# Kernel tuning notes

Measured on AMD Instinct MI355X. Metric: run time of the kernel, lower is better.

Reference implementation:

```python
import jax, jax.numpy as jnp
import numpy as np

D = 768
H = 8
DH = D // H
SCALE = DH ** -0.5


def layer_norm(x, g, b, eps=1e-5):
    mu = jnp.mean(x, axis=-1, keepdims=True)
    var = jnp.var(x, axis=-1, keepdims=True)
    return (x - mu) * jax.lax.rsqrt(var + eps) * g + b


def setup_inputs() -> dict:
    key = jax.random.key(0)
    ks = jax.random.split(key, 8)
    B, N = 8, 1024
    s = lambda fan_in: 1.0 / np.sqrt(fan_in)
    return {
        "x": jax.random.normal(ks[0], (B, N, D), jnp.float32),
        "w_qkv": jax.random.normal(ks[1], (D, 3 * D), jnp.float32) * s(D),
        "w_o": jax.random.normal(ks[2], (D, D), jnp.float32) * s(D),
        "b_o": jnp.zeros((D,), jnp.float32),
        "w1": jax.random.normal(ks[3], (D, 4 * D), jnp.float32) * s(D),
        "b1": jnp.zeros((4 * D,), jnp.float32),
        "w2": jax.random.normal(ks[4], (4 * D, D), jnp.float32) * s(4 * D),
        "b2": jnp.zeros((D,), jnp.float32),
        "g1": jnp.ones((D,), jnp.float32), "be1": jnp.zeros((D,), jnp.float32),
        "gm": jnp.ones((D,), jnp.float32), "bm": jnp.zeros((D,), jnp.float32),
        "g3": jnp.ones((D,), jnp.float32), "be3": jnp.zeros((D,), jnp.float32),
    }


def reference(x, w_qkv, w_o, b_o, w1, b1, w2, b2, g1, be1, gm, bm, g3, be3):
    B, N, _ = x.shape
    # --- attention branch (pre-norm) ---
    h = layer_norm(x, g1, be1)
    qkv = h @ w_qkv                                   # (B,N,3D)
    qkv = qkv.reshape(B, N, 3, H, DH).transpose(2, 0, 3, 1, 4)  # (3,B,H,N,Dh)
    q, k, v = qkv[0], qkv[1], qkv[2]
    att = jax.nn.softmax(jnp.einsum('bhnd,bhmd->bhnm', q, k) * SCALE, axis=-1)
    o = jnp.einsum('bhnm,bhmd->bhnd', att, v)         # (B,H,N,Dh)
    # faithful to original: reshape WITHOUT transposing heads back
    o = o.reshape(B, N, D)
    o = o @ w_o + b_o
    x = o + x
    # --- MLP branch (has its own pre-norm; GELU after BOTH linears; dropout off) ---
    h = layer_norm(x, gm, bm)
    h = jax.nn.gelu(h @ w1 + b1, approximate=False)
    h = jax.nn.gelu(h @ w2 + b2, approximate=False)
    x = h + x
    return layer_norm(x, g3, be3)
```

## Files before the change

kernel.cpp:

```cpp
#include <hip/hip_runtime.h>
#include <cmath>
#include <cstdint>

typedef __bf16 bf16;
typedef __bf16 bf16x8 __attribute__((ext_vector_type(8)));
typedef __bf16 bf16x4 __attribute__((ext_vector_type(4)));
typedef float  f32x4  __attribute__((ext_vector_type(4)));

#define M_TOK 8192
#define SCALE_ 0.10206207261596575f

__device__ __forceinline__ void gld_lds16(const void* g, void* l) {
  __builtin_amdgcn_global_load_lds(
      (__attribute__((address_space(1))) void*)(uintptr_t)g,
      (__attribute__((address_space(3))) void*)(uintptr_t)l,
      16, 0, 0);
}

__device__ __forceinline__ float gelu_f(float x) {
  float u = x * (0.7978845608f + 0.0356774081f * x * x);
  float t = 1.0f - 2.0f / (__expf(2.0f * u) + 1.0f);
  return 0.5f * x * (1.0f + t);
}

__global__ __launch_bounds__(256) void make_frags_kernel(
    const float* __restrict__ w_qkv, const float* __restrict__ w_o,
    const float* __restrict__ w1, const float* __restrict__ w2,
    bf16* __restrict__ fqkv, bf16* __restrict__ fwo, bf16* __restrict__ fw1,
    bf16* __restrict__ fw2) {
  int chunk = blockIdx.x * 4 + (threadIdx.x >> 6);
  int lane = threadIdx.x & 63;
  const float* src;
  bf16* dst;
  int K, N, base;
  if (chunk < 3456) {
    src = w_qkv; dst = fqkv; K = 768; N = 2304; base = 0;
  } else if (chunk < 4608) {
    src = w_o; dst = fwo; K = 768; N = 768; base = 3456;
  } else if (chunk < 9216) {
    src = w1; dst = fw1; K = 768; N = 3072; base = 4608;
  } else {
    src = w2; dst = fw2; K = 3072; N = 768; base = 9216;
  }
  int lid = chunk - base;
  int kc = K / 32;
  int n16 = lid / kc, c = lid - n16 * kc;
  int lr = lane & 15, qd = lane >> 4;
  int n = n16 * 16 + lr;
  int k0 = c * 32 + qd * 8;
  bf16x8 v;
#pragma unroll
  for (int e = 0; e < 8; e++) v[e] = (bf16)src[(size_t)(k0 + e) * N + n];
  *(bf16x8*)&dst[(size_t)lid * 512 + lane * 8] = v;
}

__global__ __launch_bounds__(256) void ln_kernel(
    const float* __restrict__ x, const float* __restrict__ g,
    const float* __restrict__ b, bf16* __restrict__ ob) {
  int w = threadIdx.x >> 6, lane = threadIdx.x & 63;
  size_t row = (size_t)blockIdx.x * 4 + w;
  const float* xr = x + row * 768;
  float4 v[3];
  float s = 0.f, sq = 0.f;
#pragma unroll
  for (int k = 0; k < 3; k++) {
    v[k] = *(const float4*)(xr + (k * 64 + lane) * 4);
    s += v[k].x + v[k].y + v[k].z + v[k].w;
    sq += v[k].x * v[k].x + v[k].y * v[k].y + v[k].z * v[k].z + v[k].w * v[k].w;
  }
#pragma unroll
  for (int off = 32; off >= 1; off >>= 1) {
    s += __shfl_xor(s, off);
    sq += __shfl_xor(sq, off);
  }
  float mean = s * (1.f / 768.f);
  float rstd = rsqrtf(sq * (1.f / 768.f) - mean * mean + 1e-5f);
#pragma unroll
  for (int k = 0; k < 3; k++) {
    int c = (k * 64 + lane) * 4;
    float4 gg = *(const float4*)(g + c);
    float4 bb = *(const float4*)(b + c);
    bf16x4 pk = {(bf16)((v[k].x - mean) * rstd * gg.x + bb.x),
                 (bf16)((v[k].y - mean) * rstd * gg.y + bb.y),
                 (bf16)((v[k].z - mean) * rstd * gg.z + bb.z),
                 (bf16)((v[k].w - mean) * rstd * gg.w + bb.w)};
    *(bf16x4*)(ob + row * 768 + c) = pk;
  }
}

__global__ __launch_bounds__(256) void ln2_reduce_kernel(
    const bf16* __restrict__ p, const float* __restrict__ bo,
    const float* __restrict__ xres, const float* __restrict__ g,
    const float* __restrict__ b, bf16* __restrict__ x2,
    bf16* __restrict__ h2) {
  int w = threadIdx.x >> 6, lane = threadIdx.x & 63;
  size_t row = (size_t)blockIdx.x * 4 + w;
  const bf16* p0 = p + row * 768;
  const bf16* p1 = p0 + (size_t)M_TOK * 768;
  const float* xr = xres + row * 768;
  float4 v[3];
  float s = 0.f, sq = 0.f;
#pragma unroll
  for (int k = 0; k < 3; k++) {
    int c = (k * 64 + lane) * 4;
    bf16x4 a0 = *(const bf16x4*)(p0 + c);
    bf16x4 a1 = *(const bf16x4*)(p1 + c);
    float4 bb = *(const float4*)(bo + c);
    float4 rr = *(const float4*)(xr + c);
    v[k].x = (float)a0[0] + (float)a1[0] + bb.x + rr.x;
    v[k].y = (float)a0[1] + (float)a1[1] + bb.y + rr.y;
    v[k].z = (float)a0[2] + (float)a1[2] + bb.z + rr.z;
    v[k].w = (float)a0[3] + (float)a1[3] + bb.w + rr.w;
    bf16x4 xo = {(bf16)v[k].x, (bf16)v[k].y, (bf16)v[k].z, (bf16)v[k].w};
    *(bf16x4*)(x2 + row * 768 + c) = xo;
    s += v[k].x + v[k].y + v[k].z + v[k].w;
    sq += v[k].x * v[k].x + v[k].y * v[k].y + v[k].z * v[k].z + v[k].w * v[k].w;
  }
#pragma unroll
  for (int off = 32; off >= 1; off >>= 1) {
    s += __shfl_xor(s, off);
    sq += __shfl_xor(sq, off);
  }
  float mean = s * (1.f / 768.f);
  float rstd = rsqrtf(sq * (1.f / 768.f) - mean * mean + 1e-5f);
#pragma unroll
  for (int k = 0; k < 3; k++) {
    int c = (k * 64 + lane) * 4;
    float4 gg = *(const float4*)(g + c);
    float4 bb = *(const float4*)(b + c);
    bf16x4 pk = {(bf16)((v[k].x - mean) * rstd * gg.x + bb.x),
                 (bf16)((v[k].y - mean) * rstd * gg.y + bb.y),
                 (bf16)((v[k].z - mean) * rstd * gg.z + bb.z),
                 (bf16)((v[k].w - mean) * rstd * gg.w + bb.w)};
    *(bf16x4*)(h2 + row * 768 + c) = pk;
  }
}

__global__ __launch_bounds__(256) void ln3_reduce_kernel(
    const bf16* __restrict__ p, const float* __restrict__ b2,
    const bf16* __restrict__ x2, const float* __restrict__ g,
    const float* __restrict__ b, float* __restrict__ out) {
  int w = threadIdx.x >> 6, lane = threadIdx.x & 63;
  size_t row = (size_t)blockIdx.x * 4 + w;
  const bf16* p0 = p + row * 768;
  const bf16* p1 = p0 + (size_t)M_TOK * 768;
  const bf16* xr = x2 + row * 768;
  float4 v[3];
  float s = 0.f, sq = 0.f;
#pragma unroll
  for (int k = 0; k < 3; k++) {
    int c = (k * 64 + lane) * 4;
    bf16x4 a0 = *(const bf16x4*)(p0 + c);
    bf16x4 a1 = *(const bf16x4*)(p1 + c);
    float4 bb = *(const float4*)(b2 + c);
    bf16x4 rr = *(const bf16x4*)(xr + c);
    v[k].x = gelu_f((float)a0[0] + (float)a1[0] + bb.x) + (float)rr[0];
    v[k].y = gelu_f((float)a0[1] + (float)a1[1] + bb.y) + (float)rr[1];
    v[k].z = gelu_f((float)a0[2] + (float)a1[2] + bb.z) + (float)rr[2];
    v[k].w = gelu_f((float)a0[3] + (float)a1[3] + bb.w) + (float)rr[3];
    s += v[k].x + v[k].y + v[k].z + v[k].w;
    sq += v[k].x * v[k].x + v[k].y * v[k].y + v[k].z * v[k].z + v[k].w * v[k].w;
  }
#pragma unroll
  for (int off = 32; off >= 1; off >>= 1) {
    s += __shfl_xor(s, off);
    sq += __shfl_xor(sq, off);
  }
  float mean = s * (1.f / 768.f);
  float rstd = rsqrtf(sq * (1.f / 768.f) - mean * mean + 1e-5f);
#pragma unroll
  for (int k = 0; k < 3; k++) {
    int c = (k * 64 + lane) * 4;
    float4 gg = *(const float4*)(g + c);
    float4 bb = *(const float4*)(b + c);
    float4 ov = {(v[k].x - mean) * rstd * gg.x + bb.x,
                 (v[k].y - mean) * rstd * gg.y + bb.y,
                 (v[k].z - mean) * rstd * gg.z + bb.z,
                 (v[k].w - mean) * rstd * gg.w + bb.w};
    *(float4*)(out + row * 768 + c) = ov;
  }
}

template <int EPI, int LDA, int KT, int KSL, int NN>
__global__ __launch_bounds__(256) void gemm_bt_kernel(
    const bf16* __restrict__ A, const bf16* __restrict__ Bf,
    const float* __restrict__ bias, bf16* __restrict__ outb,
    bf16* __restrict__ qo, bf16* __restrict__ ko, bf16* __restrict__ vto) {
  __shared__ __align__(16) bf16 As[2][128 * 32];
  int tid = threadIdx.x;
  int wave = tid >> 6, lane = tid & 63;
  int qd = lane >> 4, lr = lane & 15;
  int bm0 = blockIdx.x * 128, bn0 = blockIdx.y * 128;
  int wm = (wave >> 1) * 64, wn = (wave & 1) * 64;
  int kbase = blockIdx.z * KSL;
  const int STEPS = KSL / 32;
  const int KC = KT / 32;

  f32x4 acc[4][4] = {};

  int srow = lane >> 2;
  int scol = ((lane & 3) ^ ((lane >> 3) & 3)) * 8;
  const bf16* Ag = A + (size_t)(bm0 + wave * 32 + srow) * LDA + kbase + scol;
  const bf16* Ag2 = Ag + (size_t)16 * LDA;
  int rk = (lr >> 1) & 3;

  const bf16* Bfb =
      Bf + ((size_t)((bn0 + wn) >> 4) * KC + (kbase >> 5)) * 512 + lane * 8;

  auto stage = [&](int c, int buf) {
    char* Al = (char*)As[buf] + wave * 2048;
    gld_lds16(Ag + c * 32, Al);
    gld_lds16(Ag2 + c * 32, Al + 1024);
  };

  stage(0, 0);
  int cur = 0;
#pragma unroll 4
  for (int c = 0; c < STEPS; c++) {
    __syncthreads();
    if (c + 1 < STEPS) stage(c + 1, cur ^ 1);
    bf16x8 breg[4];
#pragma unroll
    for (int jn = 0; jn < 4; jn++)
      breg[jn] = *(const bf16x8*)(Bfb + ((size_t)jn * KC + c) * 512);
    const bf16* Asr = As[cur];
    bf16x8 af[4];
#pragma unroll
    for (int i = 0; i < 4; i++)
      af[i] = *(const bf16x8*)&Asr[(wm + i * 16 + lr) * 32 + ((qd ^ rk) * 8)];
#pragma unroll
    for (int i = 0; i < 4; i++)
#pragma unroll
      for (int j = 0; j < 4; j++)
        acc[i][j] = __builtin_amdgcn_mfma_f32_16x16x32_bf16(af[i], breg[j],
                                                            acc[i][j], 0, 0, 0);
    cur ^= 1;
  }

  bf16* outbs = (EPI == 5) ? outb + (size_t)blockIdx.z * M_TOK * NN : outb;

#pragma unroll
  for (int i = 0; i < 4; i++) {
#pragma unroll
    for (int j = 0; j < 4; j++) {
      if (EPI == 4) {
        int colt = bn0 + wn + j * 16;
        int which = colt / 768;
        int rem = colt - which * 768;
        int h = rem / 96;
        int dhb = rem - h * 96;
        int row0 = bm0 + wm + i * 16 + qd * 4;
        int b = row0 >> 10, n0 = row0 & 1023;
        int bh = b * 8 + h;
        if (which == 2) {
          bf16x4 pk = {(bf16)acc[i][j][0], (bf16)acc[i][j][1],
                       (bf16)acc[i][j][2], (bf16)acc[i][j][3]};
          *(bf16x4*)(vto + ((size_t)(bh * 96 + dhb + lr)) * 1024 + n0) = pk;
        } else if (which == 0) {
#pragma unroll
          for (int r = 0; r < 4; r++)
            qo[((size_t)bh * 1024 + n0 + r) * 96 + dhb + lr] =
                (bf16)(acc[i][j][r] * SCALE_);
        } else {
#pragma unroll
          for (int r = 0; r < 4; r++)
            ko[((size_t)bh * 1024 + n0 + r) * 96 + dhb + lr] =
                (bf16)acc[i][j][r];
        }
      } else {
#pragma unroll
        for (int r = 0; r < 4; r++) {
          int row = bm0 + wm + i * 16 + qd * 4 + r;
          int col = bn0 + wn + j * 16 + lr;
          size_t o = (size_t)row * NN + col;
          float v = acc[i][j][r];
          if (EPI == 2) {
            outbs[o] = (bf16)gelu_f(v + bias[col]);
          } else {
            outbs[o] = (bf16)v;
          }
        }
      }
    }
  }
}

__global__ __launch_bounds__(256) void attn_kernel(
    const bf16* __restrict__ qb, const bf16* __restrict__ kb,
    const bf16* __restrict__ vtb, bf16* __restrict__ operm) {
  __shared__ __align__(16) bf16 Ks[2][64 * 104];
  __shared__ __align__(16) bf16 Vs[2][96 * 72];
  __shared__ __align__(16) bf16 Ps[128 * 72];
  int t = threadIdx.x;
  int w = t >> 6, lane = t & 63;
  int qd = lane >> 4, lr = lane & 15;
  int bh = blockIdx.x, nt0 = blockIdx.y * 128;
  int bq = bh >> 3, hh = bh & 7;

  const bf16* kgb = kb + (size_t)bh * 1024 * 96;
  const bf16* vgb = vtb + (size_t)bh * 96 * 1024;

  bf16x8 kreg[3], vreg[3];
#pragma unroll
  for (int it = 0; it < 3; it++) {
    int idx = it * 256 + t;
    kreg[it] = *(const bf16x8*)(kgb + (idx / 12) * 96 + (idx % 12) * 8);
    vreg[it] = *(const bf16x8*)(vgb + (size_t)(idx >> 3) * 1024 + (idx & 7) * 8);
  }

  const bf16* qg = qb + ((size_t)bh * 1024 + nt0 + w * 32) * 96;
  bf16x8 afq[2][3];
#pragma unroll
  for (int i = 0; i < 2; i++)
#pragma unroll
    for (int ks = 0; ks < 3; ks++)
      afq[i][ks] = *(const bf16x8*)(qg + (i * 16 + lr) * 96 + ks * 32 + qd * 8);

  f32x4 oacc[2][6] = {};
  float lst[2][4] = {};

  int cur = 0;
  for (int kt = 0; kt < 16; kt++) {
#pragma unroll
    for (int it = 0; it < 3; it++) {
      int idx = it * 256 + t;
      *(bf16x8*)&Ks[cur][(idx / 12) * 104 + (idx % 12) * 8] = kreg[it];
      *(bf16x8*)&Vs[cur][(idx >> 3) * 72 + (idx & 7) * 8] = vreg[it];
    }
    if (kt < 15) {
      const bf16* kg = kgb + (size_t)(kt + 1) * 64 * 96;
      const bf16* vg = vgb + (kt + 1) * 64;
#pragma unroll
      for (int it = 0; it < 3; it++) {
        int idx = it * 256 + t;
        kreg[it] = *(const bf16x8*)(kg + (idx / 12) * 96 + (idx % 12) * 8);
        vreg[it] =
            *(const bf16x8*)(vg + (size_t)(idx >> 3) * 1024 + (idx & 7) * 8);
      }
    }
    __syncthreads();

    f32x4 sacc[2][4] = {};
#pragma unroll
    for (int ks = 0; ks < 3; ks++) {
      bf16x8 bk[4];
#pragma unroll
      for (int jn = 0; jn < 4; jn++)
        bk[jn] =
            *(const bf16x8*)&Ks[cur][(jn * 16 + lr) * 104 + ks * 32 + qd * 8];
#pragma unroll
      for (int i = 0; i < 2; i++)
#pragma unroll
        for (int jn = 0; jn < 4; jn++)
          sacc[i][jn] = __builtin_amdgcn_mfma_f32_16x16x32_bf16(
              afq[i][ks], bk[jn], sacc[i][jn], 0, 0, 0);
    }

#pragma unroll
    for (int i = 0; i < 2; i++)
#pragma unroll
      for (int jn = 0; jn < 4; jn++)
#pragma unroll
        for (int r = 0; r < 4; r++) {
          float p = __expf(sacc[i][jn][r]);
          lst[i][r] += p;
          Ps[(w * 32 + i * 16 + qd * 4 + r) * 72 + jn * 16 + lr] = (bf16)p;
        }

#pragma unroll
    for (int ks = 0; ks < 2; ks++) {
      bf16x8 ap[2];
#pragma unroll
      for (int i = 0; i < 2; i++)
        ap[i] =
            *(const bf16x8*)&Ps[(w * 32 + i * 16 + lr) * 72 + ks * 32 + qd * 8];
#pragma unroll
      for (int jn = 0; jn < 6; jn++) {
        bf16x8 bv =
            *(const bf16x8*)&Vs[cur][(jn * 16 + lr) * 72 + ks * 32 + qd * 8];
#pragma unroll
        for (int i = 0; i < 2; i++)
          oacc[i][jn] = __builtin_amdgcn_mfma_f32_16x16x32_bf16(
              ap[i], bv, oacc[i][jn], 0, 0, 0);
      }
    }
    cur ^= 1;
  }

#pragma unroll
  for (int i = 0; i < 2; i++)
#pragma unroll
    for (int r = 0; r < 4; r++) {
#pragma unroll
      for (int off = 1; off < 16; off <<= 1)
        lst[i][r] += __shfl_xor(lst[i][r], off);
    }

#pragma unroll
  for (int i = 0; i < 2; i++) {
#pragma unroll
    for (int r = 0; r < 4; r++) {
      float inv = 1.0f / lst[i][r];
      int n = nt0 + w * 32 + i * 16 + qd * 4 + r;
      size_t rowo = (size_t)bq * 1024 + hh * 128 + (n >> 3);
      int colb = 96 * (n & 7);
#pragma unroll
      for (int jn = 0; jn < 6; jn++)
        operm[rowo * 768 + colb + jn * 16 + lr] =
            (bf16)(oacc[i][jn][r] * inv);
    }
  }
}

extern "C" void kernel_launch(void* const* d_in, const int* in_sizes, int n_in,
                              void* d_out, int out_size, void* d_ws,
                              size_t ws_size, hipStream_t stream) {
  const float* x = (const float*)d_in[0];
  const float* w_qkv = (const float*)d_in[1];
  const float* w_o = (const float*)d_in[2];
  const float* b_o = (const float*)d_in[3];
  const float* w1 = (const float*)d_in[4];
  const float* b1 = (const float*)d_in[5];
  const float* w2 = (const float*)d_in[6];
  const float* b2 = (const float*)d_in[7];
  const float* g1 = (const float*)d_in[8];
  const float* be1 = (const float*)d_in[9];
  const float* gm = (const float*)d_in[10];
  const float* bm = (const float*)d_in[11];
  const float* g3 = (const float*)d_in[12];
  const float* be3 = (const float*)d_in[13];

  char* ws = (char*)d_ws;
  size_t off = 0;
  auto alloc = [&](size_t bytes) {
    char* p = ws + off;
    off += (bytes + 255) & ~(size_t)255;
    return p;
  };
  const size_t SZ_TOK_BF = (size_t)M_TOK * 768 * 2;
  bf16* fqkv = (bf16*)alloc((size_t)2304 * 768 * 2);
  bf16* fwo = (bf16*)alloc((size_t)768 * 768 * 2);
  bf16* fw1 = (bf16*)alloc((size_t)3072 * 768 * 2);
  bf16* fw2 = (bf16*)alloc((size_t)768 * 3072 * 2);
  bf16* hA = (bf16*)alloc(SZ_TOK_BF);
  bf16* qb = (bf16*)alloc(SZ_TOK_BF);
  bf16* kbuf = (bf16*)alloc(SZ_TOK_BF);
  bf16* vtb = (bf16*)alloc(SZ_TOK_BF);
  bf16* x2 = (bf16*)alloc(SZ_TOK_BF);
  char* G = alloc((size_t)M_TOK * 3072 * 2);
  bf16* operm = hA;
  bf16* h2 = hA;
  bf16* pWo = (bf16*)G;
  bf16* a1 = (bf16*)G;
  bf16* pW2 = hA;

  make_frags_kernel<<<3456, 256, 0, stream>>>(w_qkv, w_o, w1, w2, fqkv, fwo,
                                              fw1, fw2);

  ln_kernel<<<M_TOK / 4, 256, 0, stream>>>(x, g1, be1, hA);

  gemm_bt_kernel<4, 768, 768, 768, 2304><<<dim3(64, 18), 256, 0, stream>>>(
      hA, fqkv, nullptr, nullptr, qb, kbuf, vtb);

  attn_kernel<<<dim3(64, 8), 256, 0, stream>>>(qb, kbuf, vtb, operm);

  gemm_bt_kernel<5, 768, 768, 384, 768><<<dim3(64, 6, 2), 256, 0, stream>>>(
      operm, fwo, nullptr, pWo, nullptr, nullptr, nullptr);

  ln2_reduce_kernel<<<M_TOK / 4, 256, 0, stream>>>(pWo, b_o, x, gm, bm, x2, h2);

  gemm_bt_kernel<2, 768, 768, 768, 3072><<<dim3(64, 24), 256, 0, stream>>>(
      h2, fw1, b1, a1, nullptr, nullptr, nullptr);

  gemm_bt_kernel<5, 3072, 3072, 1536, 768><<<dim3(64, 6, 2), 256, 0, stream>>>(
      a1, fw2, nullptr, pW2, nullptr, nullptr, nullptr);

  ln3_reduce_kernel<<<M_TOK / 4, 256, 0, stream>>>(pW2, b2, x2, g3, be3,
                                                   (float*)d_out);
}
```

Baseline: 366.7 us.

## Rewrite GEMM as 8-wave 128x256 tile with triple-buffered LDS pipeline

Replaces the 4-wave 128x128 GEMM with an 8-wave, 512-thread kernel computing 128x256 tiles over a 64-wide K step. Both A and B are staged into LDS through a three-buffer pipeline that prefetches two tiles ahead, using explicit waitcnt, barriers and s_setprio around the MFMA blocks. Previously B was read straight from global memory into registers. The aim is better operand reuse and hiding of global load latency. In exchange it uses about 144KB of LDS per block and relies on hand-tuned synchronization, and the larger tiles mean fewer blocks in the grid.

```diff
diff --git a/kernel.cpp b/kernel.cpp
--- a/kernel.cpp
+++ b/kernel.cpp
@@ -181,62 +181,102 @@
   }
 }
 
-template <int EPI, int LDA, int KT, int KSL, int NN>
-__global__ __launch_bounds__(256) void gemm_bt_kernel(
+template <int EPI, int LDA, int KTOT, int KSL, int NN>
+__global__ __launch_bounds__(512, 2) void gemm8p_kernel(
     const bf16* __restrict__ A, const bf16* __restrict__ Bf,
     const float* __restrict__ bias, bf16* __restrict__ outb,
     bf16* __restrict__ qo, bf16* __restrict__ ko, bf16* __restrict__ vto) {
-  __shared__ __align__(16) bf16 As[2][128 * 32];
+  constexpr int KCg = KTOT / 32;
+  constexpr int NT = KSL / 64;
+  __shared__ __align__(16) bf16 smem[3][24576];
   int tid = threadIdx.x;
-  int wave = tid >> 6, lane = tid & 63;
-  int qd = lane >> 4, lr = lane & 15;
-  int bm0 = blockIdx.x * 128, bn0 = blockIdx.y * 128;
-  int wm = (wave >> 1) * 64, wn = (wave & 1) * 64;
+  int w = tid >> 6, l = tid & 63;
+  int qd = l >> 4, lr = l & 15;
+  int bm0 = blockIdx.x * 128, bn0 = blockIdx.y * 256;
   int kbase = blockIdx.z * KSL;
-  const int STEPS = KSL / 32;
-  const int KC = KT / 32;
+  int wm = (w >> 2) * 64;
+  int wnl = (w & 3) * 4;
+
+  int rA = w * 8 + (l >> 3);
+  int csA = (l & 7) ^ (l >> 3);
+  const bf16* pA =
+      A + (size_t)(bm0 + rA) * LDA + kbase + csA * 8;
+  const bf16* pB0 =
+      Bf + ((size_t)((bn0 >> 4) + (w >> 1)) * KCg + (kbase >> 5) + (w & 1)) *
+               512 +
+      l * 8;
+
+  auto STG_A = [&](int t, bf16* buf) {
+    gld_lds16(pA + t * 64, (char*)buf + w * 1024);
+    gld_lds16(pA + t * 64 + (size_t)64 * LDA, (char*)buf + (8 + w) * 1024);
+  };
+  auto STG_B = [&](int t, bf16* buf, int g) {
+    gld_lds16(pB0 + (size_t)g * (4 * KCg * 512) + (size_t)t * 1024,
+              (char*)buf + 16384 + (w + 8 * g) * 1024);
+  };
+
+  STG_A(0, smem[0]);
+  STG_B(0, smem[0], 0); STG_B(0, smem[0], 1);
+  STG_B(0, smem[0], 2); STG_B(0, smem[0], 3);
+  STG_A(1, smem[1]);
+  STG_B(1, smem[1], 0); STG_B(1, smem[1], 1);
+  STG_B(1, smem[1], 2); STG_B(1, smem[1], 3);
+  asm volatile("s_waitcnt vmcnt(6)" ::: "memory");
+  __builtin_amdgcn_sched_barrier(0);
+  __builtin_amdgcn_s_barrier();
 
   f32x4 acc[4][4] = {};
 
-  int srow = lane >> 2;
-  int scol = ((lane & 3) ^ ((lane >> 3) & 3)) * 8;
-  const bf16* Ag = A + (size_t)(bm0 + wave * 32 + srow) * LDA + kbase + scol;
-  const bf16* Ag2 = Ag + (size_t)16 * LDA;
-  int rk = (lr >> 1) & 3;
-
-  const bf16* Bfb =
-      Bf + ((size_t)((bn0 + wn) >> 4) * KC + (kbase >> 5)) * 512 + lane * 8;
-
-  auto stage = [&](int c, int buf) {
-    char* Al = (char*)As[buf] + wave * 2048;
-    gld_lds16(Ag + c * 32, Al);
-    gld_lds16(Ag2 + c * 32, Al + 1024);
-  };
-
-  stage(0, 0);
-  int cur = 0;
-#pragma unroll 4
-  for (int c = 0; c < STEPS; c++) {
-    __syncthreads();
-    if (c + 1 < STEPS) stage(c + 1, cur ^ 1);
-    bf16x8 breg[4];
-#pragma unroll
-    for (int jn = 0; jn < 4; jn++)
-      breg[jn] = *(const bf16x8*)(Bfb + ((size_t)jn * KC + c) * 512);
-    const bf16* Asr = As[cur];
-    bf16x8 af[4];
-#pragma unroll
-    for (int i = 0; i < 4; i++)
-      af[i] = *(const bf16x8*)&Asr[(wm + i * 16 + lr) * 32 + ((qd ^ rk) * 8)];
-#pragma unroll
-    for (int i = 0; i < 4; i++)
-#pragma unroll
-      for (int j = 0; j < 4; j++)
-        acc[i][j] = __builtin_amdgcn_mfma_f32_16x16x32_bf16(af[i], breg[j],
-                                                            acc[i][j], 0, 0, 0);
-    cur ^= 1;
-  }
-
+#pragma unroll 1
+  for (int kt3 = 0; kt3 < NT; kt3 += 3) {
+#pragma unroll
+    for (int u = 0; u < 3; ++u) {
+      const int kt = kt3 + u;
+      const bf16* Ab = smem[u];
+      const bf16* Bb = smem[u] + 8192;
+      bf16* nbuf = smem[(u + 2) % 3];
+      bool st = (kt + 2) < NT;
+#pragma unroll
+      for (int k2 = 0; k2 < 2; ++k2) {
+        bf16x8 af[4], bv[4];
+#pragma unroll
+        for (int i = 0; i < 4; ++i)
+          af[i] = *(const bf16x8*)(Ab + (wm + i * 16 + lr) * 64 +
+                                   (((k2 << 2) | qd) ^ (lr & 7)) * 8);
+#pragma unroll
+        for (int j = 0; j < 4; ++j)
+          bv[j] = *(const bf16x8*)(Bb + (((wnl + j) << 1) | k2) * 512 + l * 8);
+        if (k2 == 0) {
+          if (st) { STG_A(kt + 2, nbuf); STG_B(kt + 2, nbuf, 0); }
+        } else {
+          if (st) {
+            STG_B(kt + 2, nbuf, 1);
+            STG_B(kt + 2, nbuf, 2);
+            STG_B(kt + 2, nbuf, 3);
+          }
+        }
+        __builtin_amdgcn_s_barrier();
+        asm volatile("s_waitcnt lgkmcnt(0)" ::: "memory");
+        __builtin_amdgcn_sched_barrier(0);
+        __builtin_amdgcn_s_setprio(1);
+#pragma unroll
+        for (int i = 0; i < 4; ++i)
+#pragma unroll
+          for (int j = 0; j < 4; ++j)
+            acc[i][j] = __builtin_amdgcn_mfma_f32_16x16x32_bf16(
+                af[i], bv[j], acc[i][j], 0, 0, 0);
+        __builtin_amdgcn_s_setprio(0);
+      }
+      if (kt + 1 < NT) {
+        if (st) asm volatile("s_waitcnt vmcnt(6)" ::: "memory");
+        else    asm volatile("s_waitcnt vmcnt(0)" ::: "memory");
+        __builtin_amdgcn_sched_barrier(0);
+        __builtin_amdgcn_s_barrier();
+      }
+    }
+  }
+
+  int wn = (w & 3) * 64;
   bf16* outbs = (EPI == 5) ? outb + (size_t)blockIdx.z * M_TOK * NN : outb;
 
 #pragma unroll
@@ -459,20 +499,20 @@
 
   ln_kernel<<<M_TOK / 4, 256, 0, stream>>>(x, g1, be1, hA);
 
-  gemm_bt_kernel<4, 768, 768, 768, 2304><<<dim3(64, 18), 256, 0, stream>>>(
+  gemm8p_kernel<4, 768, 768, 768, 2304><<<dim3(64, 9), 512, 0, stream>>>(
       hA, fqkv, nullptr, nullptr, qb, kbuf, vtb);
 
   attn_kernel<<<dim3(64, 8), 256, 0, stream>>>(qb, kbuf, vtb, operm);
 
-  gemm_bt_kernel<5, 768, 768, 384, 768><<<dim3(64, 6, 2), 256, 0, stream>>>(
+  gemm8p_kernel<5, 768, 768, 384, 768><<<dim3(64, 3, 2), 512, 0, stream>>>(
       operm, fwo, nullptr, pWo, nullptr, nullptr, nullptr);
 
   ln2_reduce_kernel<<<M_TOK / 4, 256, 0, stream>>>(pWo, b_o, x, gm, bm, x2, h2);
 
-  gemm_bt_kernel<2, 768, 768, 768, 3072><<<dim3(64, 24), 256, 0, stream>>>(
+  gemm8p_kernel<2, 768, 768, 768, 3072><<<dim3(64, 12), 512, 0, stream>>>(
       h2, fw1, b1, a1, nullptr, nullptr, nullptr);
 
-  gemm_bt_kernel<5, 3072, 3072, 1536, 768><<<dim3(64, 6, 2), 256, 0, stream>>>(
+  gemm8p_kernel<5, 3072, 3072, 1536, 768><<<dim3(64, 3, 2), 512, 0, stream>>>(
       a1, fw2, nullptr, pW2, nullptr, nullptr, nullptr);
 
   ln3_reduce_kernel<<<M_TOK / 4, 256, 0, stream>>>(pW2, b2, x2, g3, be3,
```

Result: faster. 353.4 us (-3.6%).
